# Kernel optimization log

Measured on AMD Instinct MI355X. Metric: run time of the kernel, lower is better.

Reference implementation:

```python
import jax, jax.numpy as jnp
import numpy as np

D_X = 1024
D_TEXT = 768
FUSION_DIM = D_X + D_TEXT  # 1792
M = 16
K = 2


def setup_inputs() -> dict:
    key = jax.random.key(0)
    k1, k2, k3, k4, k5 = jax.random.split(key, 5)
    B, H, W = 256, 32, 32
    x = jax.random.normal(k1, (B, D_X, H, W), dtype=jnp.float32)
    degraded = jax.random.normal(k2, (B, D_TEXT), dtype=jnp.float32)
    # learned params (random so routing is non-trivial)
    w_fusion = jax.random.normal(k3, (FUSION_DIM, FUSION_DIM), dtype=jnp.float32) * (1.0 / np.sqrt(FUSION_DIM))
    b_fusion = jax.random.normal(k4, (FUSION_DIM,), dtype=jnp.float32) * 0.01
    w_gate = jax.random.normal(k5, (FUSION_DIM, M), dtype=jnp.float32) * 0.02
    return {"x": x, "degraded": degraded, "w_fusion": w_fusion,
            "b_fusion": b_fusion, "w_gate": w_gate}


def reference(x, degraded, w_fusion, b_fusion, w_gate):
    B = x.shape[0]
    # global average pool over H,W -> [B, d_x]
    x_pooled = jnp.mean(x, axis=(2, 3))
    fused = jnp.concatenate([x_pooled, degraded], axis=1)        # [B, d_x+d_text]
    fused = jnp.dot(fused, w_fusion) + b_fusion                  # Linear
    fused = jax.nn.gelu(fused, approximate=False)                # exact GELU (torch default)
    clean_logits = jnp.dot(fused, w_gate)                        # [B, M]
    probs_for_mi = jax.nn.softmax(clean_logits, axis=1)
    # eval path: logits = clean_logits (no noise)
    num_consider = min(K + 1, M)
    top_logits, top_indices = jax.lax.top_k(clean_logits, num_consider)
    top_k_logits = top_logits[:, :K]
    top_k_indices = top_indices[:, :K]
    top_k_gates = jax.nn.softmax(top_k_logits, axis=1)
    rows = jnp.arange(B)[:, None]
    gates = jnp.zeros_like(clean_logits).at[rows, top_k_indices].set(top_k_gates)
    moe_loss = jnp.float32(0.0)
    return gates, moe_loss, probs_for_mi, top_k_indices
```

## Files before the change

### kernel.cpp

```cpp
#include <hip/hip_runtime.h>
#include <math.h>

#define D_X      1024
#define D_TEXT   768
#define FDIM     1792
#define BATCH    256
#define M_EXP    16
#define HW_TOT   1024

#define OUT_GATES 0
#define OUT_LOSS  4096
#define OUT_PROBS 4097
#define OUT_IDX   8193

#define NBLK_POOL (BATCH * D_X / 4)
#define NBLK_COPY 192

__global__ __launch_bounds__(256) void pool_copy_kernel(const float* __restrict__ x,
                                                        const float* __restrict__ deg,
                                                        float* __restrict__ fused) {
    const int blk = blockIdx.x;
    if (blk < NBLK_POOL) {
        const int gtid = blk * 256 + threadIdx.x;
        const int row  = gtid >> 6;
        const int lane = gtid & 63;
        const float4* xr = reinterpret_cast<const float4*>(x + (size_t)row * HW_TOT);
        float s = 0.0f;
#pragma unroll
        for (int k = 0; k < 4; ++k) {
            float4 v = xr[k * 64 + lane];
            s += v.x + v.y + v.z + v.w;
        }
#pragma unroll
        for (int off = 32; off > 0; off >>= 1) s += __shfl_xor(s, off, 64);
        if (lane == 0) {
            const int b = row >> 10;
            const int c = row & 1023;
            fused[(size_t)b * FDIM + c] = s * (1.0f / 1024.0f);
        }
    } else {
        const int tid = (blk - NBLK_POOL) * 256 + threadIdx.x;
        if (tid < BATCH * (D_TEXT / 4)) {
            const int b  = tid / (D_TEXT / 4);
            const int j4 = tid % (D_TEXT / 4);
            const float4 v = reinterpret_cast<const float4*>(deg)[tid];
            reinterpret_cast<float4*>(fused)[(size_t)b * (FDIM / 4) + (D_X / 4) + j4] = v;
        }
    }
}

#define BM 32
#define BN 64
#define BK 64
#define NITER (FDIM / BK)

#define LOADA(k0)                                                                     \
    pa0 = *reinterpret_cast<const float4*>(A + (size_t)(m0 + ar) * FDIM + (k0) + ak4);       \
    pa1 = *reinterpret_cast<const float4*>(A + (size_t)(m0 + ar + 16) * FDIM + (k0) + ak4);

#define LOADW(k0)                                                                     \
    pw0 = *reinterpret_cast<const float4*>(W + (size_t)((k0) + wr0) * FDIM + n0 + wc4);      \
    pw1 = *reinterpret_cast<const float4*>(W + (size_t)((k0) + wr0 + 16) * FDIM + n0 + wc4); \
    pw2 = *reinterpret_cast<const float4*>(W + (size_t)((k0) + wr0 + 32) * FDIM + n0 + wc4); \
    pw3 = *reinterpret_cast<const float4*>(W + (size_t)((k0) + wr0 + 48) * FDIM + n0 + wc4);

#define STOREA(buf)                                                                   \
    As[buf][ak4 + 0][ar] = pa0.x; As[buf][ak4 + 1][ar] = pa0.y;                       \
    As[buf][ak4 + 2][ar] = pa0.z; As[buf][ak4 + 3][ar] = pa0.w;                       \
    As[buf][ak4 + 0][ar + 16] = pa1.x; As[buf][ak4 + 1][ar + 16] = pa1.y;             \
    As[buf][ak4 + 2][ar + 16] = pa1.z; As[buf][ak4 + 3][ar + 16] = pa1.w;

#define STOREW(buf)                                                                   \
    *reinterpret_cast<float4*>(&Ws[buf][wr0][wc4])      = pw0;                        \
    *reinterpret_cast<float4*>(&Ws[buf][wr0 + 16][wc4]) = pw1;                        \
    *reinterpret_cast<float4*>(&Ws[buf][wr0 + 32][wc4]) = pw2;                        \
    *reinterpret_cast<float4*>(&Ws[buf][wr0 + 48][wc4]) = pw3;

__global__ __launch_bounds__(256) void gemm_gate_kernel(const float* __restrict__ A,
                                                        const float* __restrict__ W,
                                                        const float* __restrict__ bias,
                                                        const float* __restrict__ wg,
                                                        float* __restrict__ part) {
    __shared__ float As[2][BK][BM + 1];
    __shared__ float Ws[2][BK][BN];
    __shared__ float wgs[BN][M_EXP];
    __shared__ float actS[BM][BN + 1];

    const int tid = threadIdx.x;
    const int tx = tid & 15;
    const int ty = tid >> 4;
    const int m0 = blockIdx.x * BM;
    const int n0 = blockIdx.y * BN;

    {
        const int r  = tid >> 2;
        const int c4 = (tid & 3) * 4;
        *reinterpret_cast<float4*>(&wgs[r][c4]) =
            *reinterpret_cast<const float4*>(wg + (size_t)(n0 + r) * M_EXP + c4);
    }

    const int ar  = tid >> 4;
    const int ak4 = (tid & 15) * 4;
    const int wr0 = tid >> 4;
    const int wc4 = (tid & 15) * 4;

    float4 pa0, pa1, pw0, pw1, pw2, pw3;

    LOADA(0); LOADW(0);
    STOREA(0); STOREW(0);
    LOADA(BK); LOADW(BK);
    __syncthreads();

    float acc[2][4] = {};
    int cur = 0;

    for (int t = 0; t < NITER; ++t) {
#pragma unroll
        for (int kk = 0; kk < BK; ++kk) {
            const float2 a = *reinterpret_cast<const float2*>(&As[cur][kk][ty * 2]);
            const float4 w = *reinterpret_cast<const float4*>(&Ws[cur][kk][tx * 4]);
            acc[0][0] = fmaf(a.x, w.x, acc[0][0]);
            acc[0][1] = fmaf(a.x, w.y, acc[0][1]);
            acc[0][2] = fmaf(a.x, w.z, acc[0][2]);
            acc[0][3] = fmaf(a.x, w.w, acc[0][3]);
            acc[1][0] = fmaf(a.y, w.x, acc[1][0]);
            acc[1][1] = fmaf(a.y, w.y, acc[1][1]);
            acc[1][2] = fmaf(a.y, w.z, acc[1][2]);
            acc[1][3] = fmaf(a.y, w.w, acc[1][3]);
        }
        if (t < NITER - 1) {
            const int nxt = cur ^ 1;
            STOREA(nxt); STOREW(nxt);
            if (t < NITER - 2) {
                const int k0 = (t + 2) * BK;
                LOADA(k0); LOADW(k0);
            }
            __syncthreads();
            cur = nxt;
        }
    }

#pragma unroll
    for (int i = 0; i < 2; ++i) {
        const int m = ty * 2 + i;
#pragma unroll
        for (int j = 0; j < 4; ++j) {
            const int n = tx * 4 + j;
            const float v = acc[i][j] + bias[n0 + n];
            actS[m][n] = v * 0.5f * (1.0f + erff(v * 0.70710678118654752440f));
        }
    }
    __syncthreads();

    const int pm = tid >> 3;
    const int pe = (tid & 7) * 2;
    float s0 = 0.0f, s1 = 0.0f;
#pragma unroll
    for (int n = 0; n < BN; ++n) {
        const float a = actS[pm][n];
        s0 = fmaf(a, wgs[n][pe], s0);
        s1 = fmaf(a, wgs[n][pe + 1], s1);
    }
    float* pr = part + ((size_t)blockIdx.y * BATCH + (m0 + pm)) * M_EXP + pe;
    pr[0] = s0;
    pr[1] = s1;
}

__global__ __launch_bounds__(64) void finalize_kernel(const float* __restrict__ part,
                                                      float* __restrict__ out) {
    const int b = blockIdx.x * 64 + threadIdx.x;

    float l[M_EXP];
#pragma unroll
    for (int m = 0; m < M_EXP; ++m) l[m] = 0.0f;

    for (int nb = 0; nb < NITER; ++nb) {
        const float4* pr = reinterpret_cast<const float4*>(part + ((size_t)nb * BATCH + b) * M_EXP);
#pragma unroll
        for (int q = 0; q < 4; ++q) {
            const float4 v = pr[q];
            l[q * 4 + 0] += v.x;
            l[q * 4 + 1] += v.y;
            l[q * 4 + 2] += v.z;
            l[q * 4 + 3] += v.w;
        }
    }

    float mx = l[0];
#pragma unroll
    for (int m = 1; m < M_EXP; ++m) mx = fmaxf(mx, l[m]);
    float e[M_EXP], s = 0.0f;
#pragma unroll
    for (int m = 0; m < M_EXP; ++m) { e[m] = expf(l[m] - mx); s += e[m]; }
    const float inv = 1.0f / s;
#pragma unroll
    for (int m = 0; m < M_EXP; ++m) out[OUT_PROBS + b * M_EXP + m] = e[m] * inv;

    int i0 = 0; float v0 = l[0];
#pragma unroll
    for (int m = 1; m < M_EXP; ++m) if (l[m] > v0) { v0 = l[m]; i0 = m; }
    int i1 = -1; float v1 = -INFINITY;
#pragma unroll
    for (int m = 0; m < M_EXP; ++m) if (m != i0 && l[m] > v1) { v1 = l[m]; i1 = m; }

    const float t = expf(v1 - v0);
    const float g0 = 1.0f / (1.0f + t);
    const float g1 = t * g0;

#pragma unroll
    for (int m = 0; m < M_EXP; ++m) out[OUT_GATES + b * M_EXP + m] = 0.0f;
    out[OUT_GATES + b * M_EXP + i0] = g0;
    out[OUT_GATES + b * M_EXP + i1] = g1;

    out[OUT_IDX + b * 2 + 0] = (float)i0;
    out[OUT_IDX + b * 2 + 1] = (float)i1;

    if (b == 0) out[OUT_LOSS] = 0.0f;
}

extern "C" void kernel_launch(void* const* d_in, const int* in_sizes, int n_in,
                              void* d_out, int out_size, void* d_ws, size_t ws_size,
                              hipStream_t stream) {
    const float* x        = (const float*)d_in[0];
    const float* degraded = (const float*)d_in[1];
    const float* w_fusion = (const float*)d_in[2];
    const float* b_fusion = (const float*)d_in[3];
    const float* w_gate   = (const float*)d_in[4];
    float* out = (float*)d_out;

    float* fused = (float*)d_ws;
    float* part  = fused + (size_t)BATCH * FDIM;

    pool_copy_kernel<<<NBLK_POOL + NBLK_COPY, 256, 0, stream>>>(x, degraded, fused);

    gemm_gate_kernel<<<dim3(BATCH / BM, FDIM / BN), 256, 0, stream>>>(fused, w_fusion, b_fusion, w_gate, part);

    finalize_kernel<<<BATCH / 64, 64, 0, stream>>>(part, out);
}
```

Measured before the change: 250.1 us.

## Split-K GEMM with separate reduce+GELU+gate kernel and grid-stride pooling

The pooling kernel now uses a fixed grid of persistent blocks, and each wave reduces two rows per iteration. The degraded-feature copy is folded into a grid-stride loop. The fused GEMM is split along K into two halves, with 128-thread blocks computing 4x4 register tiles at BK=32, and partial results go to a workspace buffer. A new reduce kernel sums the two partials, adds the bias, applies GELU and does the gate projection, which adds one launch and one extra global round trip of the activations.

```diff
diff --git a/kernel.cpp b/kernel.cpp
--- a/kernel.cpp
+++ b/kernel.cpp
@@ -13,82 +13,151 @@
 #define OUT_PROBS 4097
 #define OUT_IDX   8193
 
-#define NBLK_POOL (BATCH * D_X / 4)
-#define NBLK_COPY 192
+#define POOL_BLOCKS 2048
+#define NROWS (BATCH * D_X)
 
 __global__ __launch_bounds__(256) void pool_copy_kernel(const float* __restrict__ x,
                                                         const float* __restrict__ deg,
                                                         float* __restrict__ fused) {
-    const int blk = blockIdx.x;
-    if (blk < NBLK_POOL) {
-        const int gtid = blk * 256 + threadIdx.x;
-        const int row  = gtid >> 6;
-        const int lane = gtid & 63;
-        const float4* xr = reinterpret_cast<const float4*>(x + (size_t)row * HW_TOT);
-        float s = 0.0f;
+    const int tid  = threadIdx.x;
+    const int lane = tid & 63;
+    const int gw   = blockIdx.x * 4 + (tid >> 6);
+
+    for (int r2 = gw * 2; r2 < NROWS; r2 += 2 * 4 * POOL_BLOCKS) {
+        const float4* x0 = reinterpret_cast<const float4*>(x + (size_t)r2 * HW_TOT);
+        float4 v0[4], v1[4];
+#pragma unroll
+        for (int k = 0; k < 4; ++k) v0[k] = x0[k * 64 + lane];
+#pragma unroll
+        for (int k = 0; k < 4; ++k) v1[k] = x0[256 + k * 64 + lane];
+        float s0 = 0.0f, s1 = 0.0f;
 #pragma unroll
         for (int k = 0; k < 4; ++k) {
-            float4 v = xr[k * 64 + lane];
-            s += v.x + v.y + v.z + v.w;
-        }
-#pragma unroll
-        for (int off = 32; off > 0; off >>= 1) s += __shfl_xor(s, off, 64);
+            s0 += v0[k].x + v0[k].y + v0[k].z + v0[k].w;
+            s1 += v1[k].x + v1[k].y + v1[k].z + v1[k].w;
+        }
+#pragma unroll
+        for (int off = 32; off > 0; off >>= 1) {
+            s0 += __shfl_xor(s0, off, 64);
+            s1 += __shfl_xor(s1, off, 64);
+        }
         if (lane == 0) {
-            const int b = row >> 10;
-            const int c = row & 1023;
-            fused[(size_t)b * FDIM + c] = s * (1.0f / 1024.0f);
-        }
-    } else {
-        const int tid = (blk - NBLK_POOL) * 256 + threadIdx.x;
-        if (tid < BATCH * (D_TEXT / 4)) {
-            const int b  = tid / (D_TEXT / 4);
-            const int j4 = tid % (D_TEXT / 4);
-            const float4 v = reinterpret_cast<const float4*>(deg)[tid];
-            reinterpret_cast<float4*>(fused)[(size_t)b * (FDIM / 4) + (D_X / 4) + j4] = v;
-        }
+            const int b = r2 >> 10;
+            const int c = r2 & 1023;
+            float2 st;
+            st.x = s0 * (1.0f / 1024.0f);
+            st.y = s1 * (1.0f / 1024.0f);
+            *reinterpret_cast<float2*>(&fused[(size_t)b * FDIM + c]) = st;
+        }
+    }
+
+    for (int id = blockIdx.x * 256 + tid; id < BATCH * (D_TEXT / 4); id += POOL_BLOCKS * 256) {
+        const int b  = id / (D_TEXT / 4);
+        const int j4 = id % (D_TEXT / 4);
+        reinterpret_cast<float4*>(fused)[(size_t)b * (FDIM / 4) + (D_X / 4) + j4] =
+            reinterpret_cast<const float4*>(deg)[id];
     }
 }
 
 #define BM 32
 #define BN 64
-#define BK 64
-#define NITER (FDIM / BK)
-
-#define LOADA(k0)                                                                     \
-    pa0 = *reinterpret_cast<const float4*>(A + (size_t)(m0 + ar) * FDIM + (k0) + ak4);       \
-    pa1 = *reinterpret_cast<const float4*>(A + (size_t)(m0 + ar + 16) * FDIM + (k0) + ak4);
-
-#define LOADW(k0)                                                                     \
-    pw0 = *reinterpret_cast<const float4*>(W + (size_t)((k0) + wr0) * FDIM + n0 + wc4);      \
-    pw1 = *reinterpret_cast<const float4*>(W + (size_t)((k0) + wr0 + 16) * FDIM + n0 + wc4); \
-    pw2 = *reinterpret_cast<const float4*>(W + (size_t)((k0) + wr0 + 32) * FDIM + n0 + wc4); \
-    pw3 = *reinterpret_cast<const float4*>(W + (size_t)((k0) + wr0 + 48) * FDIM + n0 + wc4);
-
-#define STOREA(buf)                                                                   \
-    As[buf][ak4 + 0][ar] = pa0.x; As[buf][ak4 + 1][ar] = pa0.y;                       \
-    As[buf][ak4 + 2][ar] = pa0.z; As[buf][ak4 + 3][ar] = pa0.w;                       \
-    As[buf][ak4 + 0][ar + 16] = pa1.x; As[buf][ak4 + 1][ar + 16] = pa1.y;             \
-    As[buf][ak4 + 2][ar + 16] = pa1.z; As[buf][ak4 + 3][ar + 16] = pa1.w;
-
-#define STOREW(buf)                                                                   \
-    *reinterpret_cast<float4*>(&Ws[buf][wr0][wc4])      = pw0;                        \
-    *reinterpret_cast<float4*>(&Ws[buf][wr0 + 16][wc4]) = pw1;                        \
-    *reinterpret_cast<float4*>(&Ws[buf][wr0 + 32][wc4]) = pw2;                        \
-    *reinterpret_cast<float4*>(&Ws[buf][wr0 + 48][wc4]) = pw3;
-
-__global__ __launch_bounds__(256) void gemm_gate_kernel(const float* __restrict__ A,
-                                                        const float* __restrict__ W,
-                                                        const float* __restrict__ bias,
-                                                        const float* __restrict__ wg,
-                                                        float* __restrict__ part) {
-    __shared__ float As[2][BK][BM + 1];
+#define BK 32
+#define KSPLIT 2
+#define KPB (FDIM / KSPLIT)
+#define NIT (KPB / BK)
+
+#define LOADA(k0)                                                                         \
+    pa[0] = *reinterpret_cast<const float4*>(A + (size_t)(m0 + ar) * FDIM + (k0) + ak4);  \
+    pa[1] = *reinterpret_cast<const float4*>(A + (size_t)(m0 + ar + 16) * FDIM + (k0) + ak4);
+
+#define LOADW(k0)                                                                              \
+    pw[0] = *reinterpret_cast<const float4*>(W + (size_t)((k0) + wr) * FDIM + n0 + wc4);       \
+    pw[1] = *reinterpret_cast<const float4*>(W + (size_t)((k0) + wr + 8) * FDIM + n0 + wc4);   \
+    pw[2] = *reinterpret_cast<const float4*>(W + (size_t)((k0) + wr + 16) * FDIM + n0 + wc4);  \
+    pw[3] = *reinterpret_cast<const float4*>(W + (size_t)((k0) + wr + 24) * FDIM + n0 + wc4);
+
+#define STOREA(b)                                                                 \
+    As[b][ak4 + 0][ar] = pa[0].x; As[b][ak4 + 1][ar] = pa[0].y;                   \
+    As[b][ak4 + 2][ar] = pa[0].z; As[b][ak4 + 3][ar] = pa[0].w;                   \
+    As[b][ak4 + 0][ar + 16] = pa[1].x; As[b][ak4 + 1][ar + 16] = pa[1].y;         \
+    As[b][ak4 + 2][ar + 16] = pa[1].z; As[b][ak4 + 3][ar + 16] = pa[1].w;
+
+#define STOREW(b)                                                                 \
+    *reinterpret_cast<float4*>(&Ws[b][wr][wc4])      = pw[0];                     \
+    *reinterpret_cast<float4*>(&Ws[b][wr + 8][wc4])  = pw[1];                     \
+    *reinterpret_cast<float4*>(&Ws[b][wr + 16][wc4]) = pw[2];                     \
+    *reinterpret_cast<float4*>(&Ws[b][wr + 24][wc4]) = pw[3];
+
+__global__ __launch_bounds__(128) void gemm_split_kernel(const float* __restrict__ A,
+                                                         const float* __restrict__ W,
+                                                         float* __restrict__ pact) {
+    __shared__ float As[2][BK][BM + 4];
     __shared__ float Ws[2][BK][BN];
+
+    const int tid = threadIdx.x;
+    const int tx  = tid & 15;
+    const int ty  = tid >> 4;
+    const int m0  = blockIdx.x * BM;
+    const int n0  = blockIdx.y * BN;
+    const int kz  = blockIdx.z * KPB;
+
+    const int ar  = tid >> 3;
+    const int ak4 = (tid & 7) * 4;
+    const int wr  = tid >> 4;
+    const int wc4 = (tid & 15) * 4;
+
+    float4 pa[2], pw[4];
+
+    LOADA(kz); LOADW(kz);
+    STOREA(0); STOREW(0);
+    LOADA(kz + BK); LOADW(kz + BK);
+    __syncthreads();
+
+    float acc[4][4] = {};
+    int cur = 0;
+
+    for (int t = 0; t < NIT; ++t) {
+#pragma unroll
+        for (int kk = 0; kk < BK; ++kk) {
+            const float4 a = *reinterpret_cast<const float4*>(&As[cur][kk][ty * 4]);
+            const float4 w = *reinterpret_cast<const float4*>(&Ws[cur][kk][tx * 4]);
+            const float av[4] = {a.x, a.y, a.z, a.w};
+            const float wv[4] = {w.x, w.y, w.z, w.w};
+#pragma unroll
+            for (int i = 0; i < 4; ++i)
+#pragma unroll
+                for (int j = 0; j < 4; ++j)
+                    acc[i][j] = fmaf(av[i], wv[j], acc[i][j]);
+        }
+        if (t < NIT - 1) {
+            const int nxt = cur ^ 1;
+            STOREA(nxt); STOREW(nxt);
+            if (t < NIT - 2) {
+                const int k0 = kz + (t + 2) * BK;
+                LOADA(k0); LOADW(k0);
+            }
+            __syncthreads();
+            cur = nxt;
+        }
+    }
+
+    float* o = pact + ((size_t)blockIdx.z * BATCH + m0 + ty * 4) * FDIM + n0 + tx * 4;
+#pragma unroll
+    for (int i = 0; i < 4; ++i) {
+        float4 v;
+        v.x = acc[i][0]; v.y = acc[i][1]; v.z = acc[i][2]; v.w = acc[i][3];
+        *reinterpret_cast<float4*>(o + (size_t)i * FDIM) = v;
+    }
+}
+
+__global__ __launch_bounds__(256) void reduce_gate_kernel(const float* __restrict__ pact,
+                                                          const float* __restrict__ bias,
+                                                          const float* __restrict__ wg,
+                                                          float* __restrict__ part) {
+    __shared__ float actS[BM][BN + 1];
     __shared__ float wgs[BN][M_EXP];
-    __shared__ float actS[BM][BN + 1];
 
     const int tid = threadIdx.x;
-    const int tx = tid & 15;
-    const int ty = tid >> 4;
     const int m0 = blockIdx.x * BM;
     const int n0 = blockIdx.y * BN;
 
@@ -99,56 +168,20 @@
             *reinterpret_cast<const float4*>(wg + (size_t)(n0 + r) * M_EXP + c4);
     }
 
-    const int ar  = tid >> 4;
-    const int ak4 = (tid & 15) * 4;
-    const int wr0 = tid >> 4;
-    const int wc4 = (tid & 15) * 4;
-
-    float4 pa0, pa1, pw0, pw1, pw2, pw3;
-
-    LOADA(0); LOADW(0);
-    STOREA(0); STOREW(0);
-    LOADA(BK); LOADW(BK);
-    __syncthreads();
-
-    float acc[2][4] = {};
-    int cur = 0;
-
-    for (int t = 0; t < NITER; ++t) {
-#pragma unroll
-        for (int kk = 0; kk < BK; ++kk) {
-            const float2 a = *reinterpret_cast<const float2*>(&As[cur][kk][ty * 2]);
-            const float4 w = *reinterpret_cast<const float4*>(&Ws[cur][kk][tx * 4]);
-            acc[0][0] = fmaf(a.x, w.x, acc[0][0]);
-            acc[0][1] = fmaf(a.x, w.y, acc[0][1]);
-            acc[0][2] = fmaf(a.x, w.z, acc[0][2]);
-            acc[0][3] = fmaf(a.x, w.w, acc[0][3]);
-            acc[1][0] = fmaf(a.y, w.x, acc[1][0]);
-            acc[1][1] = fmaf(a.y, w.y, acc[1][1]);
-            acc[1][2] = fmaf(a.y, w.z, acc[1][2]);
-            acc[1][3] = fmaf(a.y, w.w, acc[1][3]);
-        }
-        if (t < NITER - 1) {
-            const int nxt = cur ^ 1;
-            STOREA(nxt); STOREW(nxt);
-            if (t < NITER - 2) {
-                const int k0 = (t + 2) * BK;
-                LOADA(k0); LOADW(k0);
-            }
-            __syncthreads();
-            cur = nxt;
-        }
-    }
-
-#pragma unroll
-    for (int i = 0; i < 2; ++i) {
-        const int m = ty * 2 + i;
-#pragma unroll
-        for (int j = 0; j < 4; ++j) {
-            const int n = tx * 4 + j;
-            const float v = acc[i][j] + bias[n0 + n];
-            actS[m][n] = v * 0.5f * (1.0f + erff(v * 0.70710678118654752440f));
-        }
+    const int row = tid >> 3;
+    const int c8  = (tid & 7) * 8;
+    const size_t base = (size_t)(m0 + row) * FDIM + n0 + c8;
+#pragma unroll
+    for (int h = 0; h < 2; ++h) {
+        const float4 p0 = *reinterpret_cast<const float4*>(pact + base + h * 4);
+        const float4 p1 = *reinterpret_cast<const float4*>(pact + (size_t)BATCH * FDIM + base + h * 4);
+        const float4 bb = *reinterpret_cast<const float4*>(bias + n0 + c8 + h * 4);
+        const float vv[4] = {p0.x + p1.x + bb.x, p0.y + p1.y + bb.y,
+                             p0.z + p1.z + bb.z, p0.w + p1.w + bb.w};
+#pragma unroll
+        for (int j = 0; j < 4; ++j)
+            actS[row][c8 + h * 4 + j] =
+                vv[j] * 0.5f * (1.0f + erff(vv[j] * 0.70710678118654752440f));
     }
     __syncthreads();
 
@@ -161,10 +194,12 @@
         s0 = fmaf(a, wgs[n][pe], s0);
         s1 = fmaf(a, wgs[n][pe + 1], s1);
     }
-    float* pr = part + ((size_t)blockIdx.y * BATCH + (m0 + pm)) * M_EXP + pe;
+    float* pr = part + ((size_t)blockIdx.y * BATCH + m0 + pm) * M_EXP + pe;
     pr[0] = s0;
     pr[1] = s1;
 }
+
+#define NNB (FDIM / BN)
 
 __global__ __launch_bounds__(64) void finalize_kernel(const float* __restrict__ part,
                                                       float* __restrict__ out) {
@@ -174,7 +209,7 @@
 #pragma unroll
     for (int m = 0; m < M_EXP; ++m) l[m] = 0.0f;
 
-    for (int nb = 0; nb < NITER; ++nb) {
+    for (int nb = 0; nb < NNB; ++nb) {
         const float4* pr = reinterpret_cast<const float4*>(part + ((size_t)nb * BATCH + b) * M_EXP);
 #pragma unroll
         for (int q = 0; q < 4; ++q) {
@@ -229,11 +264,14 @@
     float* out = (float*)d_out;
 
     float* fused = (float*)d_ws;
-    float* part  = fused + (size_t)BATCH * FDIM;
-
-    pool_copy_kernel<<<NBLK_POOL + NBLK_COPY, 256, 0, stream>>>(x, degraded, fused);
-
-    gemm_gate_kernel<<<dim3(BATCH / BM, FDIM / BN), 256, 0, stream>>>(fused, w_fusion, b_fusion, w_gate, part);
+    float* pact  = fused + (size_t)BATCH * FDIM;
+    float* part  = pact + (size_t)KSPLIT * BATCH * FDIM;
+
+    pool_copy_kernel<<<POOL_BLOCKS, 256, 0, stream>>>(x, degraded, fused);
+
+    gemm_split_kernel<<<dim3(BATCH / BM, FDIM / BN, KSPLIT), 128, 0, stream>>>(fused, w_fusion, pact);
+
+    reduce_gate_kernel<<<dim3(BATCH / BM, FDIM / BN), 256, 0, stream>>>(pact, b_fusion, w_gate, part);
 
     finalize_kernel<<<BATCH / 64, 64, 0, stream>>>(part, out);
 }
```

Result: slower. 288.0 us (+15.2%).

## Split fusion GEMM K-range and overlap degraded-text part with pooling

Applied to the files above, without the earlier changes.

The GEMM over the concatenated input is split by K. The 768-column degraded-text part is computed by 224 extra blocks inside the pooling kernel, which run alongside the bandwidth-bound pooling of x, and its partial products go to a workspace buffer. The main GEMM then covers only the 1024 pooled columns, starting its accumulators from those partials. This removes the copy of degraded into fused and shortens the K loop of the second kernel, at the cost of writing and re-reading a 256x1792 partial buffer.

```diff
diff --git a/kernel.cpp b/kernel.cpp
--- a/kernel.cpp
+++ b/kernel.cpp
@@ -13,15 +13,22 @@
 #define OUT_PROBS 4097
 #define OUT_IDX   8193
 
-#define NBLK_POOL (BATCH * D_X / 4)
-#define NBLK_COPY 192
-
-__global__ __launch_bounds__(256) void pool_copy_kernel(const float* __restrict__ x,
-                                                        const float* __restrict__ deg,
-                                                        float* __restrict__ fused) {
-    const int blk = blockIdx.x;
-    if (blk < NBLK_POOL) {
-        const int gtid = blk * 256 + threadIdx.x;
+#define NBLK_DGEMM 224
+#define NBLK_POOL  (BATCH * D_X / 4)
+
+__global__ __launch_bounds__(256) void pool_deggemm_kernel(const float* __restrict__ x,
+                                                           const float* __restrict__ deg,
+                                                           const float* __restrict__ W,
+                                                           float* __restrict__ fused,
+                                                           float* __restrict__ pact2) {
+    __shared__ float As1[32][33];
+    __shared__ float Ws1[32][64];
+
+    const int bid = blockIdx.x;
+    const int tid = threadIdx.x;
+
+    if (bid >= NBLK_DGEMM) {
+        const int gtid = (bid - NBLK_DGEMM) * 256 + tid;
         const int row  = gtid >> 6;
         const int lane = gtid & 63;
         const float4* xr = reinterpret_cast<const float4*>(x + (size_t)row * HW_TOT);
@@ -33,30 +40,70 @@
         }
 #pragma unroll
         for (int off = 32; off > 0; off >>= 1) s += __shfl_xor(s, off, 64);
-        if (lane == 0) {
-            const int b = row >> 10;
-            const int c = row & 1023;
-            fused[(size_t)b * FDIM + c] = s * (1.0f / 1024.0f);
-        }
-    } else {
-        const int tid = (blk - NBLK_POOL) * 256 + threadIdx.x;
-        if (tid < BATCH * (D_TEXT / 4)) {
-            const int b  = tid / (D_TEXT / 4);
-            const int j4 = tid % (D_TEXT / 4);
-            const float4 v = reinterpret_cast<const float4*>(deg)[tid];
-            reinterpret_cast<float4*>(fused)[(size_t)b * (FDIM / 4) + (D_X / 4) + j4] = v;
-        }
+        if (lane == 0) fused[row] = s * (1.0f / 1024.0f);
+        return;
+    }
+
+    const int mb = bid / 28;
+    const int nb = bid % 28;
+    const int m0 = mb * 32;
+    const int n0 = nb * 64;
+
+    const int tx = tid & 15;
+    const int ty = tid >> 4;
+
+    const int ar  = tid >> 3;
+    const int ak4 = (tid & 7) * 4;
+    const int wk  = tid >> 4;
+    const int wc4 = (tid & 15) * 4;
+
+    float acc[2][4] = {};
+
+    for (int k0 = 0; k0 < D_TEXT; k0 += 32) {
+        __syncthreads();
+        {
+            const float4 a = *reinterpret_cast<const float4*>(
+                deg + (size_t)(m0 + ar) * D_TEXT + k0 + ak4);
+            As1[ak4 + 0][ar] = a.x; As1[ak4 + 1][ar] = a.y;
+            As1[ak4 + 2][ar] = a.z; As1[ak4 + 3][ar] = a.w;
+            *reinterpret_cast<float4*>(&Ws1[wk][wc4]) =
+                *reinterpret_cast<const float4*>(W + (size_t)(D_X + k0 + wk) * FDIM + n0 + wc4);
+            *reinterpret_cast<float4*>(&Ws1[wk + 16][wc4]) =
+                *reinterpret_cast<const float4*>(W + (size_t)(D_X + k0 + wk + 16) * FDIM + n0 + wc4);
+        }
+        __syncthreads();
+#pragma unroll
+        for (int kk = 0; kk < 32; ++kk) {
+            const float2 a = *reinterpret_cast<const float2*>(&As1[kk][ty * 2]);
+            const float4 w = *reinterpret_cast<const float4*>(&Ws1[kk][tx * 4]);
+            acc[0][0] = fmaf(a.x, w.x, acc[0][0]);
+            acc[0][1] = fmaf(a.x, w.y, acc[0][1]);
+            acc[0][2] = fmaf(a.x, w.z, acc[0][2]);
+            acc[0][3] = fmaf(a.x, w.w, acc[0][3]);
+            acc[1][0] = fmaf(a.y, w.x, acc[1][0]);
+            acc[1][1] = fmaf(a.y, w.y, acc[1][1]);
+            acc[1][2] = fmaf(a.y, w.z, acc[1][2]);
+            acc[1][3] = fmaf(a.y, w.w, acc[1][3]);
+        }
+    }
+
+#pragma unroll
+    for (int i = 0; i < 2; ++i) {
+        float4 v;
+        v.x = acc[i][0]; v.y = acc[i][1]; v.z = acc[i][2]; v.w = acc[i][3];
+        *reinterpret_cast<float4*>(pact2 + (size_t)(m0 + ty * 2 + i) * FDIM + n0 + tx * 4) = v;
     }
 }
 
 #define BM 32
 #define BN 64
 #define BK 64
-#define NITER (FDIM / BK)
+#define KDIM D_X
+#define NITER (KDIM / BK)
 
 #define LOADA(k0)                                                                     \
-    pa0 = *reinterpret_cast<const float4*>(A + (size_t)(m0 + ar) * FDIM + (k0) + ak4);       \
-    pa1 = *reinterpret_cast<const float4*>(A + (size_t)(m0 + ar + 16) * FDIM + (k0) + ak4);
+    pa0 = *reinterpret_cast<const float4*>(A + (size_t)(m0 + ar) * KDIM + (k0) + ak4);       \
+    pa1 = *reinterpret_cast<const float4*>(A + (size_t)(m0 + ar + 16) * KDIM + (k0) + ak4);
 
 #define LOADW(k0)                                                                     \
     pw0 = *reinterpret_cast<const float4*>(W + (size_t)((k0) + wr0) * FDIM + n0 + wc4);      \
@@ -78,6 +125,7 @@
 
 __global__ __launch_bounds__(256) void gemm_gate_kernel(const float* __restrict__ A,
                                                         const float* __restrict__ W,
+                                                        const float* __restrict__ pact2,
                                                         const float* __restrict__ bias,
                                                         const float* __restrict__ wg,
                                                         float* __restrict__ part) {
@@ -109,11 +157,19 @@
     LOADA(0); LOADW(0);
     STOREA(0); STOREW(0);
     LOADA(BK); LOADW(BK);
+
+    float acc[2][4];
+    {
+        const float4 i0 = *reinterpret_cast<const float4*>(
+            pact2 + (size_t)(m0 + ty * 2) * FDIM + n0 + tx * 4);
+        const float4 i1 = *reinterpret_cast<const float4*>(
+            pact2 + (size_t)(m0 + ty * 2 + 1) * FDIM + n0 + tx * 4);
+        acc[0][0] = i0.x; acc[0][1] = i0.y; acc[0][2] = i0.z; acc[0][3] = i0.w;
+        acc[1][0] = i1.x; acc[1][1] = i1.y; acc[1][2] = i1.z; acc[1][3] = i1.w;
+    }
     __syncthreads();
 
-    float acc[2][4] = {};
     int cur = 0;
-
     for (int t = 0; t < NITER; ++t) {
 #pragma unroll
         for (int kk = 0; kk < BK; ++kk) {
@@ -161,11 +217,13 @@
         s0 = fmaf(a, wgs[n][pe], s0);
         s1 = fmaf(a, wgs[n][pe + 1], s1);
     }
-    float* pr = part + ((size_t)blockIdx.y * BATCH + (m0 + pm)) * M_EXP + pe;
+    float* pr = part + ((size_t)blockIdx.y * BATCH + m0 + pm) * M_EXP + pe;
     pr[0] = s0;
     pr[1] = s1;
 }
 
+#define NNB (FDIM / BN)
+
 __global__ __launch_bounds__(64) void finalize_kernel(const float* __restrict__ part,
                                                       float* __restrict__ out) {
     const int b = blockIdx.x * 64 + threadIdx.x;
@@ -174,7 +232,7 @@
 #pragma unroll
     for (int m = 0; m < M_EXP; ++m) l[m] = 0.0f;
 
-    for (int nb = 0; nb < NITER; ++nb) {
+    for (int nb = 0; nb < NNB; ++nb) {
         const float4* pr = reinterpret_cast<const float4*>(part + ((size_t)nb * BATCH + b) * M_EXP);
 #pragma unroll
         for (int q = 0; q < 4; ++q) {
@@ -229,11 +287,14 @@
     float* out = (float*)d_out;
 
     float* fused = (float*)d_ws;
-    float* part  = fused + (size_t)BATCH * FDIM;
-
-    pool_copy_kernel<<<NBLK_POOL + NBLK_COPY, 256, 0, stream>>>(x, degraded, fused);
-
-    gemm_gate_kernel<<<dim3(BATCH / BM, FDIM / BN), 256, 0, stream>>>(fused, w_fusion, b_fusion, w_gate, part);
+    float* pact2 = fused + (size_t)BATCH * D_X;
+    float* part  = pact2 + (size_t)BATCH * FDIM;
+
+    pool_deggemm_kernel<<<NBLK_DGEMM + NBLK_POOL, 256, 0, stream>>>(x, degraded, w_fusion,
+                                                                   fused, pact2);
+
+    gemm_gate_kernel<<<dim3(BATCH / BM, FDIM / BN), 256, 0, stream>>>(fused, w_fusion, pact2,
+                                                                     b_fusion, w_gate, part);
 
     finalize_kernel<<<BATCH / 64, 64, 0, stream>>>(part, out);
 }
```

After: 235.2 us. 1.06x faster.
